# Performance work log

Hardware: AMD Instinct MI355X
Metric: run time of the kernel (lower is better)

Reference implementation:

```python
import jax, jax.numpy as jnp
import numpy as np
import math

B, S, D, H, L, D_OUT = 8, 1024, 1024, 16, 2, 1024
DK = D // H
LN_EPS = 1e-8


def _ln(x, g, b):
    m = jnp.mean(x, axis=-1, keepdims=True)
    var = jnp.mean((x - m) ** 2, axis=-1, keepdims=True)
    return (x - m) / jnp.sqrt(var + LN_EPS) * g + b


def setup_inputs() -> dict:
    key = jax.random.key(0)
    ks = jax.random.split(key, 16)
    s = 0.02
    return {
        "q": jax.random.normal(ks[0], (B, S, D), jnp.float32),
        "k": jax.random.normal(ks[1], (B, S, D), jnp.float32),
        "v": jax.random.normal(ks[2], (B, S, D), jnp.float32),
        "attn_mask": jnp.ones((B, S, S), jnp.int32),
        # per-layer stacked params
        "Wqkv": jax.random.normal(ks[3], (L, 3, D, D), jnp.float32) * s,  # [out,in]
        "bqkv": jnp.zeros((L, 3, D), jnp.float32),
        "Wo": jax.random.normal(ks[4], (L, D, D), jnp.float32) * s,
        "bo": jnp.zeros((L, D), jnp.float32),
        "ln1_g": jnp.ones((L, D), jnp.float32),
        "ln1_b": jnp.zeros((L, D), jnp.float32),
        "ln2_g": jnp.ones((L, D), jnp.float32),
        "ln2_b": jnp.zeros((L, D), jnp.float32),
        "Wc1": jax.random.normal(ks[5], (L, D, D), jnp.float32) * s,  # conv1d k=1 == linear
        "bc1": jnp.zeros((L, D), jnp.float32),
        "Wc2": jax.random.normal(ks[6], (L, D, D), jnp.float32) * s,
        "bc2": jnp.zeros((L, D), jnp.float32),
        "last_g": jnp.ones((D,), jnp.float32),
        "last_b": jnp.zeros((D,), jnp.float32),
        "Wfc": jax.random.normal(ks[7], (D_OUT, D), jnp.float32) * s,
        "bfc": jnp.zeros((D_OUT,), jnp.float32),
    }


def reference(q, k, v, attn_mask, Wqkv, bqkv, Wo, bo, ln1_g, ln1_b, ln2_g, ln2_b,
              Wc1, bc1, Wc2, bc2, last_g, last_b, Wfc, bfc):
    scale = 1.0 / math.sqrt(DK)
    mask = (attn_mask == 0)[:, None, :, :]  # [B,1,S,S] broadcast over heads

    def proj(x, W, b):
        # linear [out,in] then split heads -> [B,H,S,dk]
        y = jnp.einsum('bsd,od->bso', x, W) + b
        return y.reshape(B, S, H, DK).transpose(0, 2, 1, 3)

    for i in range(L):
        Q = _ln(q, ln1_g[i], ln1_b[i])
        qh = proj(Q, Wqkv[i, 0], bqkv[i, 0])
        kh = proj(k, Wqkv[i, 1], bqkv[i, 1])
        vh = proj(v, Wqkv[i, 2], bqkv[i, 2])
        scores = jnp.einsum('bhqd,bhkd->bhqk', qh, kh) * scale
        scores = jnp.clip(scores, -30.0, 30.0)
        scores = jnp.where(mask, -1e9, scores) + 1e-5
        p = jax.nn.softmax(scores, axis=-1)
        x = jnp.einsum('bhqk,bhkd->bhqd', p, vh)
        x = x.transpose(0, 2, 1, 3).reshape(B, S, D)
        x = jax.nn.relu(jnp.einsum('bsd,od->bso', x, Wo[i]) + bo[i])
        k = k + x
        k = _ln(k, ln2_g[i], ln2_b[i])
        # PointWiseFeedForward: conv2(conv1(x)) + x, kernel_size=1, no activation
        h = jnp.einsum('bsd,od->bso', k, Wc1[i]) + bc1[i]
        h = jnp.einsum('bsd,od->bso', h, Wc2[i]) + bc2[i]
        k = k + h
        q = k
        v = k
    out = _ln(k, last_g, last_b)
    return jnp.einsum('bsd,od->bso', out, Wfc) + bfc
```

## Files before the change

### kernel.cpp

```cpp
#include <hip/hip_runtime.h>

typedef __attribute__((ext_vector_type(8))) short s8x;
typedef __attribute__((ext_vector_type(4))) float f4x;
typedef unsigned short u16;
typedef unsigned int u32;

#define DEV static __device__ __forceinline__

DEV u16 f2b(float f) {
    union { float f; u32 u; } v; v.f = f;
    u32 r = v.u + 0x7FFFu + ((v.u >> 16) & 1u);
    return (u16)(r >> 16);
}

DEV float b2f(u16 x) {
    union { u32 u; float f; } v; v.u = (u32)x << 16;
    return v.f;
}

DEV u32 pk2(float lo, float hi) {
    u32 r;
    asm("v_cvt_pk_bf16_f32 %0, %1, %2" : "=v"(r) : "v"(lo), "v"(hi));
    return r;
}

DEV float exp2_raw(float x) {
    float r;
    asm("v_exp_f32 %0, %1" : "=v"(r) : "v"(x));
    return r;
}

DEV void gload16(const void* g, void* lds) {
    __builtin_amdgcn_global_load_lds(
        (const __attribute__((address_space(1))) void*)g,
        (__attribute__((address_space(3))) void*)lds, 16, 0, 0);
}

#define GK 1024
#define BM 128
#define BN 128
#define BK 64


DEV void stage_unit(const u16* __restrict__ g, char* l, int tid) {
#pragma unroll
    for (int i = 0; i < 2; ++i) {
        int db = i * 8192 + tid * 16;
        int row = db >> 7;
        int cs = ((db >> 4) & 7) ^ (row & 7);
        gload16(g + (size_t)row * 1024 + cs * 8, l + db);
    }
}

DEV s8x lds_frag(const char* Lbase, int row, int kk, int lg) {
    int cb = (kk * 64 + lg * 16) ^ ((row & 7) << 4);
    return *(const s8x*)(Lbase + row * 128 + cb);
}

template<int FLAGS, int NN>
__global__ __launch_bounds__(512, 2) void gemm8(
    const u16* __restrict__ A, const u16* __restrict__ W,
    const float* __restrict__ bias, const u16* __restrict__ res,
    float* __restrict__ outf, u16* __restrict__ outb, float scl)
{
    constexpr bool RELU = (FLAGS & 1) != 0;
    constexpr bool RES  = (FLAGS & 2) != 0;
    constexpr bool WF   = (FLAGS & 4) != 0;
    constexpr bool WB   = (FLAGS & 8) != 0;
    constexpr bool RBIA = (FLAGS & 16) != 0;

    __shared__ __attribute__((aligned(16))) u16 As[3][256 * 64];
    __shared__ __attribute__((aligned(16))) u16 Bs[3][128 * 64];

    const int tid = threadIdx.x, lane = tid & 63, wid = tid >> 6;
    const int l15 = lane & 15, lg = lane >> 4;
    const int wm = wid >> 1, wn = wid & 1;
    const int bm = blockIdx.x, bn = blockIdx.y;

    const u16* Ab = A + (size_t)bm * 256 * GK;
    const u16* Wb = W + (size_t)bn * 128 * GK;

    f4x acc[4][4];
#pragma unroll
    for (int i = 0; i < 4; ++i)
#pragma unroll
        for (int j = 0; j < 4; ++j) { f4x z = {0.f, 0.f, 0.f, 0.f}; acc[i][j] = z; }

    char* a0 = (char*)As[0]; char* a1 = (char*)As[1]; char* a2 = (char*)As[2];
    char* b0 = (char*)Bs[0]; char* b1 = (char*)Bs[1]; char* b2 = (char*)Bs[2];

    stage_unit(Ab + 0 * 64,                 a0,        tid);
    stage_unit(Ab + 128 * GK + 0 * 64,      a0 + 16384, tid);
    stage_unit(Wb + 0 * 64,                 b0,        tid);
    stage_unit(Ab + 1 * 64,                 a1,        tid);
    stage_unit(Ab + 128 * GK + 1 * 64,      a1 + 16384, tid);
    stage_unit(Wb + 1 * 64,                 b1,        tid);
    asm volatile("s_waitcnt vmcnt(6)" ::: "memory");
    __builtin_amdgcn_s_barrier();

    for (int t = 0; t < 16; ++t) {
        const bool st = (t < 14);
        s8x bfr[4][2], afr[2][2];
#pragma unroll
        for (int ni = 0; ni < 4; ++ni)
#pragma unroll
            for (int kk = 0; kk < 2; ++kk)
                bfr[ni][kk] = lds_frag(b0, wn * 64 + ni * 16 + l15, kk, lg);
#pragma unroll
        for (int mi = 0; mi < 2; ++mi)
#pragma unroll
            for (int kk = 0; kk < 2; ++kk)
                afr[mi][kk] = lds_frag(a0, wm * 64 + mi * 16 + l15, kk, lg);
        if (st) {
            stage_unit(Ab + (t + 2) * 64,            a2,         tid);
            stage_unit(Ab + 128 * GK + (t + 2) * 64, a2 + 16384, tid);
        }
        __builtin_amdgcn_s_barrier();
        asm volatile("s_waitcnt lgkmcnt(0)" ::: "memory");
        __builtin_amdgcn_sched_barrier(0);
        __builtin_amdgcn_s_setprio(1);
#pragma unroll
        for (int kk = 0; kk < 2; ++kk)
#pragma unroll
            for (int mi = 0; mi < 2; ++mi)
#pragma unroll
                for (int ni = 0; ni < 4; ++ni)
                    acc[mi][ni] = __builtin_amdgcn_mfma_f32_16x16x32_bf16(afr[mi][kk], bfr[ni][kk], acc[mi][ni], 0, 0, 0);
        __builtin_amdgcn_s_setprio(0);
        __builtin_amdgcn_s_barrier();

        s8x afr2[2][2];
#pragma unroll
        for (int mi = 0; mi < 2; ++mi)
#pragma unroll
            for (int kk = 0; kk < 2; ++kk)
                afr2[mi][kk] = lds_frag(a0, wm * 64 + (mi + 2) * 16 + l15, kk, lg);
        if (st) stage_unit(Wb + (t + 2) * 64, b2, tid);
        __builtin_amdgcn_s_barrier();
        asm volatile("s_waitcnt lgkmcnt(0)" ::: "memory");
        __builtin_amdgcn_sched_barrier(0);
        __builtin_amdgcn_s_setprio(1);
#pragma unroll
        for (int kk = 0; kk < 2; ++kk)
#pragma unroll
            for (int mi = 0; mi < 2; ++mi)
#pragma unroll
                for (int ni = 0; ni < 4; ++ni)
                    acc[mi + 2][ni] = __builtin_amdgcn_mfma_f32_16x16x32_bf16(afr2[mi][kk], bfr[ni][kk], acc[mi + 2][ni], 0, 0, 0);
        __builtin_amdgcn_s_setprio(0);
        if (st) asm volatile("s_waitcnt vmcnt(6)" ::: "memory");
        else    asm volatile("s_waitcnt vmcnt(0)" ::: "memory");
        __builtin_amdgcn_s_barrier();

        char* tA = a0; a0 = a1; a1 = a2; a2 = tA;
        char* tB = b0; b0 = b1; b1 = b2; b2 = tB;
    }

#pragma unroll
    for (int ni = 0; ni < 4; ++ni) {
        int gcol = bn * 128 + wn * 64 + ni * 16 + l15;
        float bvc = RBIA ? 0.f : bias[gcol];
#pragma unroll
        for (int mi = 0; mi < 4; ++mi) {
            int grow0 = bm * 256 + wm * 64 + mi * 16 + lg * 4;
#pragma unroll
            for (int r = 0; r < 4; ++r) {
                float bv = RBIA ? bias[grow0 + r] : bvc;
                float v = (acc[mi][ni][r] + bv) * scl;
                if (RELU) v = fmaxf(v, 0.f);
                size_t oidx = (size_t)(grow0 + r) * NN + gcol;
                if (RES) v += b2f(res[oidx]);
                if (WF) outf[oidx] = v;
                if (WB) outb[oidx] = f2b(v);
            }
        }
    }
}

__global__ __launch_bounds__(256) void gemm_z2(
    const u16* __restrict__ A0, const u16* __restrict__ W0, const float* __restrict__ b0,
    u16* __restrict__ o0, float s0,
    const u16* __restrict__ A1, const u16* __restrict__ W1, const float* __restrict__ b1,
    u16* __restrict__ o1, float s1)
{
    const int z = blockIdx.z;
    const u16* A = z ? A1 : A0;
    const u16* W = z ? W1 : W0;
    const float* bias = z ? b1 : b0;
    u16* outb = z ? o1 : o0;
    const float scl = z ? s1 : s0;

    __shared__ __attribute__((aligned(16))) u16 As[2][BM * BK];
    __shared__ __attribute__((aligned(16))) u16 Bs[2][BN * BK];

    const int tid  = threadIdx.x;
    const int lane = tid & 63;
    const int wid  = tid >> 6;
    const int wr = wid >> 1, wc = wid & 1;
    const int bm = blockIdx.x, bn = blockIdx.y;
    const int l15 = lane & 15;
    const int lg  = lane >> 4;

    const u16* Ab = A + (size_t)bm * BM * GK;
    const u16* Wb = W + (size_t)bn * BN * GK;

    const int prow = tid >> 3;
    const int pcol = (tid & 7) * 8;

    f4x acc[4][4];
#pragma unroll
    for (int i = 0; i < 4; ++i)
#pragma unroll
        for (int j = 0; j < 4; ++j) { f4x z_ = {0.f, 0.f, 0.f, 0.f}; acc[i][j] = z_; }

#pragma unroll
    for (int c = 0; c < 4; ++c) {
        int row = c * 32 + prow;
        gload16(Ab + (size_t)row * GK + pcol, &As[0][row * BK + pcol]);
    }
#pragma unroll
    for (int c = 0; c < 4; ++c) {
        int row = c * 32 + prow;
        gload16(Wb + (size_t)row * GK + pcol, &Bs[0][row * BK + pcol]);
    }

    const int nkt = GK / BK;
    int cur = 0;
    for (int kt = 0; kt < nkt; ++kt) {
        __syncthreads();
        if (kt + 1 < nkt) {
            const u16* Ak = Ab + (kt + 1) * BK;
            const u16* Wk = Wb + (kt + 1) * BK;
#pragma unroll
            for (int c = 0; c < 4; ++c) {
                int row = c * 32 + prow;
                gload16(Ak + (size_t)row * GK + pcol, &As[cur ^ 1][row * BK + pcol]);
            }
#pragma unroll
            for (int c = 0; c < 4; ++c) {
                int row = c * 32 + prow;
                gload16(Wk + (size_t)row * GK + pcol, &Bs[cur ^ 1][row * BK + pcol]);
            }
        }
        const u16* Ac = As[cur];
        const u16* Bc = Bs[cur];
#pragma unroll
        for (int kk = 0; kk < 2; ++kk) {
            s8x a[4], b[4];
#pragma unroll
            for (int mi = 0; mi < 4; ++mi)
                a[mi] = *(const s8x*)(Ac + (wr * 64 + mi * 16 + l15) * BK + kk * 32 + lg * 8);
#pragma unroll
            for (int ni = 0; ni < 4; ++ni)
                b[ni] = *(const s8x*)(Bc + (wc * 64 + ni * 16 + l15) * BK + kk * 32 + lg * 8);
#pragma unroll
            for (int mi = 0; mi < 4; ++mi)
#pragma unroll
                for (int ni = 0; ni < 4; ++ni)
                    acc[mi][ni] = __builtin_amdgcn_mfma_f32_16x16x32_bf16(a[mi], b[ni], acc[mi][ni], 0, 0, 0);
        }
        cur ^= 1;
    }

#pragma unroll
    for (int ni = 0; ni < 4; ++ni) {
        int gcol = bn * BN + wc * 64 + ni * 16 + l15;
        float bvc = bias[gcol];
#pragma unroll
        for (int mi = 0; mi < 4; ++mi) {
            int grow0 = bm * BM + wr * 64 + mi * 16 + lg * 4;
#pragma unroll
            for (int r = 0; r < 4; ++r) {
                float v = (acc[mi][ni][r] + bvc) * scl;
                outb[(size_t)(grow0 + r) * 1024 + gcol] = f2b(v);
            }
        }
    }
}

__global__ __launch_bounds__(512) void attn_kernel(
    const u16* __restrict__ Qm, const u16* __restrict__ Km, const u16* __restrict__ Vt,
    const u32* __restrict__ maskw, const u32* __restrict__ rowfl,
    u16* __restrict__ Om)
{
    const int bh = blockIdx.x;
    const int b  = bh >> 4;
    const int h  = bh & 15;
    const int qt = blockIdx.y;
    const int tid = threadIdx.x, lane = tid & 63, wid = tid >> 6;
    const int l15 = lane & 15, lg = lane >> 4;

    __shared__ __attribute__((aligned(16))) u16 Ks[3][64 * 64];
    __shared__ __attribute__((aligned(16))) u16 Vs[3][64 * 64];
    __shared__ __attribute__((aligned(16))) u16 Ps[8][16][64];
    __shared__ int anymask;

    const size_t rowbase = (size_t)b * 1024;
    const int hoff = h * 64;

    if (tid == 0) anymask = 0;

    const int so   = tid * 16;
    const int srow = so >> 7;
    const int sch  = ((so >> 4) & 7) ^ (srow & 7);
    const int vswz = (l15 & 7) << 4;

    const u16* Kbase = Km + rowbase * 1024 + hoff + (size_t)srow * 1024 + sch * 8;
    const u16* Vbase = Vt + (size_t)(hoff + srow) * 8192 + b * 1024 + sch * 8;

    char* kc0 = (char*)Ks[0]; char* kc1 = (char*)Ks[1]; char* kc2 = (char*)Ks[2];
    char* vc0 = (char*)Vs[0]; char* vc1 = (char*)Vs[1]; char* vc2 = (char*)Vs[2];

    gload16(Kbase + 0 * 64 * 1024, kc0 + so);
    gload16(Vbase + 0 * 64,        vc0 + so);
    gload16(Kbase + 1 * 64 * 1024, kc1 + so);
    gload16(Vbase + 1 * 64,        vc1 + so);

    const int qrow = qt * 128 + wid * 16 + l15;
    s8x qf[2];
#pragma unroll
    for (int kk = 0; kk < 2; ++kk)
        qf[kk] = *(const s8x*)(Qm + (rowbase + qrow) * 1024 + hoff + kk * 32 + lg * 8);

    __syncthreads();
    if (tid < 128) {
        if (rowfl[rowbase + qt * 128 + tid]) atomicOr(&anymask, 1);
    }

    f4x o[4];
#pragma unroll
    for (int d = 0; d < 4; ++d) { f4x z = {0.f, 0.f, 0.f, 0.f}; o[d] = z; }
    float lrun = 0.f;

    asm volatile("s_waitcnt vmcnt(0)" ::: "memory");
    __syncthreads();
    const int am = anymask;
    const float CLIP = 43.2808512f;

    for (int kt = 0; kt < 16; ++kt) {
        if (kt + 2 < 16) {
            gload16(Kbase + (size_t)(kt + 2) * 64 * 1024, kc2 + so);
            gload16(Vbase + (kt + 2) * 64,                vc2 + so);
        }

        f4x sc[4];
#pragma unroll
        for (int ni = 0; ni < 4; ++ni) { f4x z = {0.f, 0.f, 0.f, 0.f}; sc[ni] = z; }
        __builtin_amdgcn_s_setprio(1);
#pragma unroll
        for (int kk = 0; kk < 2; ++kk) {
#pragma unroll
            for (int ni = 0; ni < 4; ++ni) {
                int row = ni * 16 + l15;
                int cb  = (kk * 64 + lg * 16) ^ ((row & 7) << 4);
                s8x kf = *(const s8x*)(kc0 + row * 128 + cb);
                sc[ni] = __builtin_amdgcn_mfma_f32_16x16x32_bf16(kf, qf[kk], sc[ni], 0, 0, 0);
            }
        }
        __builtin_amdgcn_s_setprio(0);

        if (am) {
            int qg = qt * 128 + wid * 16 + l15;
#pragma unroll
            for (int ni = 0; ni < 4; ++ni)
#pragma unroll
                for (int r = 0; r < 4; ++r) {
                    int kcol = kt * 64 + ni * 16 + lg * 4 + r;
                    u32 wb_ = maskw[(rowbase + qg) * 32 + (kcol >> 5)];
                    if (wb_ & (1u << (kcol & 31))) sc[ni][r] = -1e9f;
                }
        }

        float s = 0.f;
#pragma unroll
        for (int ni = 0; ni < 4; ++ni)
#pragma unroll
            for (int r = 0; r < 4; ++r) {
                float p = exp2_raw(fminf(sc[ni][r], CLIP));
                sc[ni][r] = p;
                s += p;
            }
        s += __shfl_xor(s, 16);
        s += __shfl_xor(s, 32);
        lrun += s;

#pragma unroll
        for (int ni = 0; ni < 4; ++ni) {
            uint2 w; w.x = pk2(sc[ni][0], sc[ni][1]); w.y = pk2(sc[ni][2], sc[ni][3]);
            *(uint2*)((char*)&Ps[wid][l15][0] + ((ni * 32 + lg * 8) ^ vswz)) = w;
        }
        s8x pa[2];
#pragma unroll
        for (int kk = 0; kk < 2; ++kk)
            pa[kk] = *(const s8x*)((const char*)&Ps[wid][l15][0] + ((kk * 64 + lg * 16) ^ vswz));

        __builtin_amdgcn_s_setprio(1);
#pragma unroll
        for (int dt = 0; dt < 4; ++dt)
#pragma unroll
            for (int kk = 0; kk < 2; ++kk) {
                int row = dt * 16 + l15;
                int cb  = (kk * 64 + lg * 16) ^ ((row & 7) << 4);
                s8x vf = *(const s8x*)(vc0 + row * 128 + cb);
                o[dt] = __builtin_amdgcn_mfma_f32_16x16x32_bf16(pa[kk], vf, o[dt], 0, 0, 0);
            }
        __builtin_amdgcn_s_setprio(0);

        if (kt + 2 < 16)      asm volatile("s_waitcnt vmcnt(2)" ::: "memory");
        else if (kt + 1 < 16) asm volatile("s_waitcnt vmcnt(0)" ::: "memory");
        __builtin_amdgcn_s_barrier();

        char* tk = kc0; kc0 = kc1; kc1 = kc2; kc2 = tk;
        char* tv = vc0; vc0 = vc1; vc1 = vc2; vc2 = tv;
    }

    float rl = 1.f / lrun;
    float rlr[4];
#pragma unroll
    for (int r = 0; r < 4; ++r) rlr[r] = __shfl(rl, lg * 4 + r);
#pragma unroll
    for (int dt = 0; dt < 4; ++dt) {
        int gc = hoff + dt * 16 + l15;
#pragma unroll
        for (int r = 0; r < 4; ++r) {
            int gr = qt * 128 + wid * 16 + lg * 4 + r;
            Om[(rowbase + gr) * 1024 + gc] = f2b(o[dt][r] * rlr[r]);
        }
    }
}

__global__ __launch_bounds__(256) void ln_f(
    const float* __restrict__ x, const float* __restrict__ g, const float* __restrict__ bb,
    u16* __restrict__ yb)
{
    const int wid = threadIdx.x >> 6, lane = threadIdx.x & 63;
    const size_t row = (size_t)blockIdx.x * 4 + wid;
    const float* xr = x + row * 1024;
    float4 v[4];
    float s = 0.f, s2 = 0.f;
#pragma unroll
    for (int c = 0; c < 4; ++c) {
        v[c] = *(const float4*)(xr + c * 256 + lane * 4);
        s  += v[c].x + v[c].y + v[c].z + v[c].w;
        s2 += v[c].x * v[c].x + v[c].y * v[c].y + v[c].z * v[c].z + v[c].w * v[c].w;
    }
#pragma unroll
    for (int m = 32; m >= 1; m >>= 1) { s += __shfl_xor(s, m); s2 += __shfl_xor(s2, m); }
    float mean = s * (1.f / 1024.f);
    float var  = s2 * (1.f / 1024.f) - mean * mean;
    float rs = rsqrtf(var + 1e-8f);
#pragma unroll
    for (int c = 0; c < 4; ++c) {
        int col = c * 256 + lane * 4;
        float4 gv = *(const float4*)(g + col);
        float4 bv = *(const float4*)(bb + col);
        ushort4 o4 = make_ushort4(
            f2b((v[c].x - mean) * rs * gv.x + bv.x),
            f2b((v[c].y - mean) * rs * gv.y + bv.y),
            f2b((v[c].z - mean) * rs * gv.z + bv.z),
            f2b((v[c].w - mean) * rs * gv.w + bv.w));
        *(ushort4*)(yb + row * 1024 + col) = o4;
    }
}

__global__ __launch_bounds__(256) void ln_b(
    const u16* __restrict__ x, const float* __restrict__ g, const float* __restrict__ bb,
    u16* __restrict__ yb)
{
    const int wid = threadIdx.x >> 6, lane = threadIdx.x & 63;
    const size_t row = (size_t)blockIdx.x * 4 + wid;
    const u16* xr = x + row * 1024 + lane * 16;
    s8x v0 = *(const s8x*)xr;
    s8x v1 = *(const s8x*)(xr + 8);
    float f[16];
    float s = 0.f, s2 = 0.f;
#pragma unroll
    for (int j = 0; j < 8; ++j) { f[j] = b2f((u16)v0[j]); f[8 + j] = b2f((u16)v1[j]); }
#pragma unroll
    for (int j = 0; j < 16; ++j) { s += f[j]; s2 += f[j] * f[j]; }
#pragma unroll
    for (int m = 32; m >= 1; m >>= 1) { s += __shfl_xor(s, m); s2 += __shfl_xor(s2, m); }
    float mean = s * (1.f / 1024.f);
    float var  = s2 * (1.f / 1024.f) - mean * mean;
    float rs = rsqrtf(var + 1e-8f);
    const int col0 = lane * 16;
    u16 ov[16];
#pragma unroll
    for (int c = 0; c < 4; ++c) {
        float4 gv = *(const float4*)(g + col0 + c * 4);
        float4 bv = *(const float4*)(bb + col0 + c * 4);
        ov[c * 4 + 0] = f2b((f[c * 4 + 0] - mean) * rs * gv.x + bv.x);
        ov[c * 4 + 1] = f2b((f[c * 4 + 1] - mean) * rs * gv.y + bv.y);
        ov[c * 4 + 2] = f2b((f[c * 4 + 2] - mean) * rs * gv.z + bv.z);
        ov[c * 4 + 3] = f2b((f[c * 4 + 3] - mean) * rs * gv.w + bv.w);
    }
    u16* yr = yb + row * 1024 + col0;
    *(ushort4*)(yr + 0)  = make_ushort4(ov[0], ov[1], ov[2], ov[3]);
    *(ushort4*)(yr + 4)  = make_ushort4(ov[4], ov[5], ov[6], ov[7]);
    *(ushort4*)(yr + 8)  = make_ushort4(ov[8], ov[9], ov[10], ov[11]);
    *(ushort4*)(yr + 12) = make_ushort4(ov[12], ov[13], ov[14], ov[15]);
}

__global__ __launch_bounds__(256) void cvt_kernel(const float* __restrict__ x, u16* __restrict__ y, int n4)
{
    int i = blockIdx.x * 256 + threadIdx.x;
    if (i < n4) {
        float4 v = *(const float4*)(x + (size_t)i * 4);
        ushort4 o = make_ushort4(f2b(v.x), f2b(v.y), f2b(v.z), f2b(v.w));
        *(ushort4*)(y + (size_t)i * 4) = o;
    }
}

__global__ __launch_bounds__(256) void cvtT_kernel(const float* __restrict__ X, u16* __restrict__ Y)
{
    __shared__ u16 T[64][65];
    const int l = blockIdx.z;
    const int j0 = blockIdx.y * 64;
    const int i0 = blockIdx.x * 64;
    const float* Xl = X + (size_t)l * 1024 * 1024;
    u16* Yl = Y + (size_t)l * 1024 * 1024;
    const int tr = threadIdx.x >> 4;
    const int tc = threadIdx.x & 15;
#pragma unroll
    for (int k = 0; k < 4; ++k) {
        int j = tr + k * 16;
        float4 v = *(const float4*)(Xl + (size_t)(j0 + j) * 1024 + i0 + tc * 4);
        T[tc * 4 + 0][j] = f2b(v.x);
        T[tc * 4 + 1][j] = f2b(v.y);
        T[tc * 4 + 2][j] = f2b(v.z);
        T[tc * 4 + 3][j] = f2b(v.w);
    }
    __syncthreads();
    const int wr_ = threadIdx.x >> 3;
    const int wc_ = threadIdx.x & 7;
#pragma unroll
    for (int k = 0; k < 2; ++k) {
        int i = wr_ + k * 32;
        u16 tmp[8];
#pragma unroll
        for (int e = 0; e < 8; ++e) tmp[e] = T[i][wc_ * 8 + e];
        *(ushort4*)(Yl + (size_t)(i0 + i) * 1024 + j0 + wc_ * 8)     = make_ushort4(tmp[0], tmp[1], tmp[2], tmp[3]);
        *(ushort4*)(Yl + (size_t)(i0 + i) * 1024 + j0 + wc_ * 8 + 4) = make_ushort4(tmp[4], tmp[5], tmp[6], tmp[7]);
    }
}

__global__ __launch_bounds__(256) void matvec_kernel(const float* __restrict__ W2, const float* __restrict__ b1,
                                                     const float* __restrict__ b2, float* __restrict__ outv)
{
    const int wid = threadIdx.x >> 6, lane = threadIdx.x & 63;
    int row = blockIdx.x * 4 + wid;
    int l = row >> 10, o = row & 1023;
    const float* wr_ = W2 + (size_t)l * 1024 * 1024 + (size_t)o * 1024;
    const float* b1l = b1 + l * 1024;
    float s = 0.f;
#pragma unroll
    for (int c = 0; c < 4; ++c) {
        float4 w = *(const float4*)(wr_ + c * 256 + lane * 4);
        float4 bv = *(const float4*)(b1l + c * 256 + lane * 4);
        s += w.x * bv.x + w.y * bv.y + w.z * bv.z + w.w * bv.w;
    }
#pragma unroll
    for (int m = 32; m >= 1; m >>= 1) s += __shfl_xor(s, m);
    if (lane == 0) outv[row] = s + b2[l * 1024 + o];
}

__global__ __launch_bounds__(256) void mask_kernel(const int* __restrict__ am, u32* __restrict__ mw)
{
    size_t idx = (size_t)blockIdx.x * 256 + threadIdx.x;
    unsigned long long bal = __ballot(am[idx] == 0);
    int lane = threadIdx.x & 63;
    if (lane == 0)  mw[idx >> 5] = (u32)bal;
    if (lane == 32) mw[idx >> 5] = (u32)(bal >> 32);
}

__global__ __launch_bounds__(256) void rowflag_kernel(const u32* __restrict__ mw, u32* __restrict__ rf)
{
    int r = blockIdx.x * 256 + threadIdx.x;
    u32 o = 0;
#pragma unroll
    for (int i = 0; i < 32; ++i) o |= mw[r * 32 + i];
    rf[r] = o;
}

extern "C" void kernel_launch(void* const* d_in, const int* in_sizes, int n_in,
                              void* d_out, int out_size, void* d_ws, size_t ws_size,
                              hipStream_t stream)
{
    (void)in_sizes; (void)n_in; (void)out_size; (void)ws_size;

    const float* q_in  = (const float*)d_in[0];
    const float* k_in  = (const float*)d_in[1];
    const float* v_in  = (const float*)d_in[2];
    const int*   amask = (const int*)d_in[3];
    const float* Wqkv  = (const float*)d_in[4];
    const float* bqkv  = (const float*)d_in[5];
    const float* Wo    = (const float*)d_in[6];
    const float* bo    = (const float*)d_in[7];
    const float* ln1g  = (const float*)d_in[8];
    const float* ln1b  = (const float*)d_in[9];
    const float* ln2g  = (const float*)d_in[10];
    const float* ln2b  = (const float*)d_in[11];
    const float* Wc1   = (const float*)d_in[12];
    const float* bc1   = (const float*)d_in[13];
    const float* Wc2   = (const float*)d_in[14];
    const float* bc2   = (const float*)d_in[15];
    const float* lastg = (const float*)d_in[16];
    const float* lastb = (const float*)d_in[17];
    const float* Wfc   = (const float*)d_in[18];
    const float* bfc   = (const float*)d_in[19];
    float* out = (float*)d_out;

    char* base = (char*)d_ws;
    size_t off = 0;
    auto alloc = [&](size_t bytes) -> char* {
        char* p = base + off;
        off = (off + bytes + 255) & ~(size_t)255;
        return p;
    };
    const size_t M1 = 1024 * 1024;
    const size_t MT = 8192 * 1024;
    u16* wqkv_b = (u16*)alloc(6 * M1 * 2);
    u16* wo_b   = (u16*)alloc(2 * M1 * 2);
    u16* wcomb  = (u16*)alloc(2 * M1 * 2);
    u16* wfc_b  = (u16*)alloc(M1 * 2);
    float* bcomb = (float*)alloc(2 * 1024 * 4);
    float* zb    = (float*)alloc(1024 * 4);
    u32* maskw  = (u32*)alloc(8192 * 32 * 4);
    u32* rowfl  = (u32*)alloc(8192 * 4);
    u16* t0 = (u16*)alloc(MT * 2);
    u16* t1 = (u16*)alloc(MT * 2);
    u16* qh = (u16*)alloc(MT * 2);
    u16* kh = (u16*)alloc(MT * 2);
    u16* vt = (u16*)alloc(MT * 2);
    u16* xb = (u16*)alloc(MT * 2);
    u16* x2 = (u16*)alloc(MT * 2);
    u16* wc1t  = qh;
    u16* wc2_b = kh;

    cvt_kernel<<<6 * M1 / 1024, 256, 0, stream>>>(Wqkv, wqkv_b, (int)(6 * M1 / 4));
    cvt_kernel<<<2 * M1 / 1024, 256, 0, stream>>>(Wo,   wo_b,   (int)(2 * M1 / 4));
    cvt_kernel<<<M1 / 1024, 256, 0, stream>>>(Wfc, wfc_b, (int)(M1 / 4));
    cvt_kernel<<<2 * M1 / 1024, 256, 0, stream>>>(Wc2, wc2_b, (int)(2 * M1 / 4));
    cvtT_kernel<<<dim3(16, 16, 2), 256, 0, stream>>>(Wc1, wc1t);
    hipMemsetAsync(zb, 0, 1024 * 4, stream);
    gemm_z2<<<dim3(8, 8, 2), 256, 0, stream>>>(
        wc2_b, wc1t, zb, wcomb, 1.f,
        wc2_b + M1, wc1t + M1, zb, wcomb + M1, 1.f);
    matvec_kernel<<<512, 256, 0, stream>>>(Wc2, bc1, bc2, bcomb);
    mask_kernel<<<32768, 256, 0, stream>>>(amask, maskw);
    rowflag_kernel<<<32, 256, 0, stream>>>(maskw, rowfl);

    dim3 g8(8192 / 256, 1024 / 128);
    dim3 v8(1024 / 256, 8192 / 128);
    const float QS = 0.125f * 1.44269504f;
    const int D = 1024;
    for (int i = 0; i < 2; ++i) {
        if (i == 0) {
            ln_f<<<2048, 256, 0, stream>>>(q_in, ln1g, ln1b, t0);
            cvt_kernel<<<8192, 256, 0, stream>>>(k_in, x2, (int)(MT / 4));
            cvt_kernel<<<8192, 256, 0, stream>>>(v_in, xb, (int)(MT / 4));
        } else {
            ln_b<<<2048, 256, 0, stream>>>(x2, ln1g + i * D, ln1b + i * D, t0);
        }
        gemm8<8, 1024><<<g8, 512, 0, stream>>>(t0, wqkv_b + (size_t)(i * 3 + 0) * M1,
                                               bqkv + (i * 3 + 0) * D, nullptr, nullptr, qh, QS);
        gemm8<8, 1024><<<g8, 512, 0, stream>>>(x2, wqkv_b + (size_t)(i * 3 + 1) * M1,
                                               bqkv + (i * 3 + 1) * D, nullptr, nullptr, kh, 1.f);
        const u16* vin_b = (i == 0) ? xb : x2;
        gemm8<8 | 16, 8192><<<v8, 512, 0, stream>>>(wqkv_b + (size_t)(i * 3 + 2) * M1, vin_b,
                                                    bqkv + (i * 3 + 2) * D, nullptr, nullptr, vt, 1.f);
        attn_kernel<<<dim3(128, 8), 512, 0, stream>>>(qh, kh, vt, maskw, rowfl, t0);
        gemm8<1 | 2 | 8, 1024><<<g8, 512, 0, stream>>>(t0, wo_b + (size_t)i * M1,
                                                       bo + i * D, x2, nullptr, t1, 1.f);
        ln_b<<<2048, 256, 0, stream>>>(t1, ln2g + i * D, ln2b + i * D, xb);
        gemm8<2 | 8, 1024><<<g8, 512, 0, stream>>>(xb, wcomb + (size_t)i * M1,
                                                   bcomb + i * 1024, xb, nullptr, x2, 1.f);
    }
    ln_b<<<2048, 256, 0, stream>>>(x2, lastg, lastb, t0);
    gemm8<4, 1024><<<g8, 512, 0, stream>>>(t0, wfc_b, bfc, nullptr, out, nullptr, 1.f);
}
```

Before: 504.6 us.

## Fuse Q and K projections into one 256x256-tile GEMM launch

Replaces the two separate 256x128-tile GEMM launches for the Q and K projections with a single launch that uses blockIdx.z to pick the operand set. Each block computes a 256x256 output tile, with triple-buffered A and double-buffered B in LDS. It splits the M-dimension MFMA work into two halves so global loads overlap with compute. The goal is more reuse per loaded tile and one fewer launch, at the cost of higher LDS use (160KB) and more accumulator registers, which may reduce occupancy.

```diff
diff --git a/kernel.cpp b/kernel.cpp
--- a/kernel.cpp
+++ b/kernel.cpp
@@ -172,6 +172,132 @@
                 if (RES) v += b2f(res[oidx]);
                 if (WF) outf[oidx] = v;
                 if (WB) outb[oidx] = f2b(v);
+            }
+        }
+    }
+}
+
+__global__ __launch_bounds__(512, 2) void gemm_qk256(
+    const u16* __restrict__ A0p, const u16* __restrict__ W0p, const float* __restrict__ b0p,
+    u16* __restrict__ o0p, float s0,
+    const u16* __restrict__ A1p, const u16* __restrict__ W1p, const float* __restrict__ b1p,
+    u16* __restrict__ o1p, float s1)
+{
+    const int z = blockIdx.z;
+    const u16* A = z ? A1p : A0p;
+    const u16* W = z ? W1p : W0p;
+    const float* bias = z ? b1p : b0p;
+    u16* outb = z ? o1p : o0p;
+    const float scl = z ? s1 : s0;
+
+    __shared__ __attribute__((aligned(16))) u16 As[3][256 * 64];
+    __shared__ __attribute__((aligned(16))) u16 Bs[2][256 * 64];
+
+    const int tid = threadIdx.x, lane = tid & 63, wid = tid >> 6;
+    const int l15 = lane & 15, lg = lane >> 4;
+    const int wm = wid >> 2;
+    const int wn = wid & 3;
+    const int bm = blockIdx.x, bn = blockIdx.y;
+
+    const u16* Ab = A + (size_t)bm * 256 * GK;
+    const u16* Wb = W + (size_t)bn * 256 * GK;
+
+    f4x acc[8][4];
+#pragma unroll
+    for (int i = 0; i < 8; ++i)
+#pragma unroll
+        for (int j = 0; j < 4; ++j) { f4x zz = {0.f, 0.f, 0.f, 0.f}; acc[i][j] = zz; }
+
+    char* a0 = (char*)As[0]; char* a1 = (char*)As[1]; char* a2 = (char*)As[2];
+    char* b0 = (char*)Bs[0]; char* b1 = (char*)Bs[1];
+
+    stage_unit(Ab + 0 * 64,            a0,         tid);
+    stage_unit(Ab + 128 * GK + 0 * 64, a0 + 16384, tid);
+    stage_unit(Wb + 0 * 64,            b0,         tid);
+    stage_unit(Wb + 128 * GK + 0 * 64, b0 + 16384, tid);
+    stage_unit(Ab + 1 * 64,            a1,         tid);
+    stage_unit(Ab + 128 * GK + 1 * 64, a1 + 16384, tid);
+    asm volatile("s_waitcnt vmcnt(4)" ::: "memory");
+    __builtin_amdgcn_s_barrier();
+
+    const char* aW = nullptr;
+    const char* bW = nullptr;
+    for (int t = 0; t < 16; ++t) {
+        aW = a0 + wm * 16384;
+        bW = b0 + (wn >> 1) * 16384;
+        const int brow0 = (wn & 1) * 64;
+
+        s8x bfr[4][2], afr[4][2];
+#pragma unroll
+        for (int ni = 0; ni < 4; ++ni)
+#pragma unroll
+            for (int kk = 0; kk < 2; ++kk)
+                bfr[ni][kk] = lds_frag(bW, brow0 + ni * 16 + l15, kk, lg);
+#pragma unroll
+        for (int mi = 0; mi < 4; ++mi)
+#pragma unroll
+            for (int kk = 0; kk < 2; ++kk)
+                afr[mi][kk] = lds_frag(aW, mi * 16 + l15, kk, lg);
+        if (t + 1 < 16) {
+            stage_unit(Wb + (t + 1) * 64,            b1,         tid);
+            stage_unit(Wb + 128 * GK + (t + 1) * 64, b1 + 16384, tid);
+        }
+        __builtin_amdgcn_s_barrier();
+        asm volatile("s_waitcnt lgkmcnt(0)" ::: "memory");
+        __builtin_amdgcn_sched_barrier(0);
+        __builtin_amdgcn_s_setprio(1);
+#pragma unroll
+        for (int kk = 0; kk < 2; ++kk)
+#pragma unroll
+            for (int mi = 0; mi < 4; ++mi)
+#pragma unroll
+                for (int ni = 0; ni < 4; ++ni)
+                    acc[mi][ni] = __builtin_amdgcn_mfma_f32_16x16x32_bf16(afr[mi][kk], bfr[ni][kk], acc[mi][ni], 0, 0, 0);
+        __builtin_amdgcn_s_setprio(0);
+        __builtin_amdgcn_s_barrier();
+
+        s8x afr2[4][2];
+#pragma unroll
+        for (int mi = 0; mi < 4; ++mi)
+#pragma unroll
+            for (int kk = 0; kk < 2; ++kk)
+                afr2[mi][kk] = lds_frag(aW, (mi + 4) * 16 + l15, kk, lg);
+        if (t + 2 < 16) {
+            stage_unit(Ab + (t + 2) * 64,            a2,         tid);
+            stage_unit(Ab + 128 * GK + (t + 2) * 64, a2 + 16384, tid);
+        }
+        __builtin_amdgcn_s_barrier();
+        asm volatile("s_waitcnt lgkmcnt(0)" ::: "memory");
+        __builtin_amdgcn_sched_barrier(0);
+        __builtin_amdgcn_s_setprio(1);
+#pragma unroll
+        for (int kk = 0; kk < 2; ++kk)
+#pragma unroll
+            for (int mi = 0; mi < 4; ++mi)
+#pragma unroll
+                for (int ni = 0; ni < 4; ++ni)
+                    acc[mi + 4][ni] = __builtin_amdgcn_mfma_f32_16x16x32_bf16(afr2[mi][kk], bfr[ni][kk], acc[mi + 4][ni], 0, 0, 0);
+        __builtin_amdgcn_s_setprio(0);
+
+        if (t <= 13)      asm volatile("s_waitcnt vmcnt(4)" ::: "memory");
+        else if (t == 14) asm volatile("s_waitcnt vmcnt(0)" ::: "memory");
+        __builtin_amdgcn_s_barrier();
+
+        char* tA = a0; a0 = a1; a1 = a2; a2 = tA;
+        char* tB = b0; b0 = b1; b1 = tB;
+    }
+
+#pragma unroll
+    for (int ni = 0; ni < 4; ++ni) {
+        int gcol = bn * 256 + wn * 64 + ni * 16 + l15;
+        float bvc = bias[gcol];
+#pragma unroll
+        for (int mi = 0; mi < 8; ++mi) {
+            int grow0 = bm * 256 + wm * 128 + mi * 16 + lg * 4;
+#pragma unroll
+            for (int r = 0; r < 4; ++r) {
+                float v = (acc[mi][ni][r] + bvc) * scl;
+                outb[(size_t)(grow0 + r) * 1024 + gcol] = f2b(v);
             }
         }
     }
@@ -652,6 +778,7 @@
 
     dim3 g8(8192 / 256, 1024 / 128);
     dim3 v8(1024 / 256, 8192 / 128);
+    dim3 gqk(8192 / 256, 1024 / 256, 2);
     const float QS = 0.125f * 1.44269504f;
     const int D = 1024;
     for (int i = 0; i < 2; ++i) {
@@ -662,10 +789,9 @@
         } else {
             ln_b<<<2048, 256, 0, stream>>>(x2, ln1g + i * D, ln1b + i * D, t0);
         }
-        gemm8<8, 1024><<<g8, 512, 0, stream>>>(t0, wqkv_b + (size_t)(i * 3 + 0) * M1,
-                                               bqkv + (i * 3 + 0) * D, nullptr, nullptr, qh, QS);
-        gemm8<8, 1024><<<g8, 512, 0, stream>>>(x2, wqkv_b + (size_t)(i * 3 + 1) * M1,
-                                               bqkv + (i * 3 + 1) * D, nullptr, nullptr, kh, 1.f);
+        gemm_qk256<<<gqk, 512, 0, stream>>>(
+            t0, wqkv_b + (size_t)(i * 3 + 0) * M1, bqkv + (i * 3 + 0) * D, qh, QS,
+            x2, wqkv_b + (size_t)(i * 3 + 1) * M1, bqkv + (i * 3 + 1) * D, kh, 1.f);
         const u16* vin_b = (i == 0) ? xb : x2;
         gemm8<8 | 16, 8192><<<v8, 512, 0, stream>>>(wqkv_b + (size_t)(i * 3 + 2) * M1, vin_b,
                                                     bqkv + (i * 3 + 2) * D, nullptr, nullptr, vt, 1.f);
```

Result: faster. 493.7 us (-2.2%).
